# Optimization experiments

Measured on AMD Instinct MI355X. Metric: run time of the kernel, lower is better.

The kernel has to match this reference:

```python
import jax, jax.numpy as jnp
import numpy as np

B, L, ENC, DEC, ATT = 256, 196, 2048, 512, 512


def setup_inputs() -> dict:
    key = jax.random.key(0)
    ks = jax.random.split(key, 10)
    s = lambda d: 1.0 / np.sqrt(d)
    return {
        "x": jax.random.normal(ks[0], (B, L, ENC), dtype=jnp.float32),
        "h": jax.random.normal(ks[1], (B, DEC), dtype=jnp.float32),
        "W_enc": jax.random.uniform(ks[2], (ENC, ATT), jnp.float32, -s(ENC), s(ENC)),
        "b_enc": jax.random.uniform(ks[3], (ATT,), jnp.float32, -s(ENC), s(ENC)),
        "W_dec": jax.random.uniform(ks[4], (DEC, ATT), jnp.float32, -s(DEC), s(DEC)),
        "b_dec": jax.random.uniform(ks[5], (ATT,), jnp.float32, -s(DEC), s(DEC)),
        "W_full": jax.random.uniform(ks[6], (ATT, 1), jnp.float32, -s(ATT), s(ATT)),
        "b_full": jax.random.uniform(ks[7], (1,), jnp.float32, -s(ATT), s(ATT)),
        "W_beta": jax.random.uniform(ks[8], (DEC, 1), jnp.float32, -s(DEC), s(DEC)),
        "b_beta": jax.random.uniform(ks[9], (1,), jnp.float32, -s(DEC), s(DEC)),
    }


def reference(x, h, W_enc, b_enc, W_dec, b_dec, W_full, b_full, W_beta, b_beta):
    # x: [B, L, ENC], h: [B, DEC]
    att1 = jnp.einsum("blc,ca->bla", x, W_enc) + b_enc          # [B, L, ATT]
    att2 = h @ W_dec + b_dec                                     # [B, ATT]
    att = (jax.nn.relu(att1 + att2[:, None, :]) @ W_full)[..., 0] + b_full  # [B, L]
    alpha = jax.nn.softmax(att, axis=-1)                         # [B, L]
    z = jnp.einsum("bl,blc->bc", alpha, x)                       # [B, ENC]
    gate_beta = jax.nn.sigmoid(h @ W_beta + b_beta)              # [B, 1]
    return gate_beta * z, alpha
```

## Files before the change

### kernel.cpp

```cpp
#include <hip/hip_runtime.h>
#include <hip/hip_bf16.h>
#include <cstdint>

#define B_   256
#define L_   196
#define ENC_ 2048
#define DEC_ 512
#define ATT_ 512
#define M_TOT (B_*L_)

typedef short short8 __attribute__((ext_vector_type(8)));
typedef float f32x16 __attribute__((ext_vector_type(16)));

__device__ __forceinline__ unsigned short f2bf(float f) {
    union { float f; unsigned u; } v; v.f = f;
    unsigned u = v.u;
    return (unsigned short)((u + 0x7FFFu + ((u >> 16) & 1u)) >> 16);
}

__device__ __forceinline__ void gl_lds16(const void* g, void* l) {
    __builtin_amdgcn_global_load_lds((const __attribute__((address_space(1))) unsigned int*)g,
                                     (__attribute__((address_space(3))) unsigned int*)l,
                                     16, 0, 0);
}

__global__ void k_transpose(const float* __restrict__ W, unsigned short* __restrict__ WT) {
    __shared__ float S[32*33];
    const int k0 = blockIdx.x * 32, n0 = blockIdx.y * 32;
    const int t  = threadIdx.x;
    const int c31 = t & 31, q = t >> 5;
#pragma unroll
    for (int i = 0; i < 4; ++i) {
        int kl = q + i*8;
        S[c31*33 + kl] = W[(size_t)(k0+kl)*ATT_ + n0 + c31];
    }
    __syncthreads();
#pragma unroll
    for (int i = 0; i < 4; ++i) {
        int nn = q + i*8;
        WT[(size_t)(n0+nn)*ENC_ + k0 + c31] = f2bf(S[nn*33 + c31]);
    }
}

__global__ void k_prep2(const float* __restrict__ h, const float* __restrict__ Wdec,
                        const float* __restrict__ bdec, const float* __restrict__ benc,
                        const float* __restrict__ Wbeta, const float* __restrict__ bbeta,
                        float* __restrict__ att2c, float* __restrict__ gate) {
    const int b = blockIdx.x, t = threadIdx.x;
    __shared__ float hs[DEC_];
    __shared__ float pr[4];
    hs[t]       = h[(size_t)b*DEC_ + t];
    hs[t + 256] = h[(size_t)b*DEC_ + t + 256];
    __syncthreads();
    float a0 = 0.f, a1 = 0.f;
    for (int k = 0; k < DEC_; ++k) {
        float hk = hs[k];
        a0 = fmaf(hk, Wdec[(size_t)k*ATT_ + t],       a0);
        a1 = fmaf(hk, Wdec[(size_t)k*ATT_ + t + 256], a1);
    }
    att2c[(size_t)b*ATT_ + t]       = a0 + bdec[t]       + benc[t];
    att2c[(size_t)b*ATT_ + t + 256] = a1 + bdec[t + 256] + benc[t + 256];
    float p = hs[t]*Wbeta[t] + hs[t+256]*Wbeta[t+256];
#pragma unroll
    for (int mask = 32; mask; mask >>= 1) p += __shfl_xor(p, mask, 64);
    if ((t & 63) == 0) pr[t >> 6] = p;
    __syncthreads();
    if (t == 0) gate[b] = 1.f / (1.f + __expf(-(pr[0]+pr[1]+pr[2]+pr[3] + bbeta[0])));
}

__global__ __launch_bounds__(256, 2) void k_gemm(
        const float* __restrict__ x, const unsigned short* __restrict__ WT,
        const float* __restrict__ att2c, const float* __restrict__ Wfull,
        float* __restrict__ att) {
    __shared__ alignas(16) unsigned short Ab[2][64*32];
    __shared__ alignas(16) unsigned short Bb[2][512*32];
    __shared__ float att_ws[4][64];

    const int tid   = threadIdx.x;
    const int wave  = tid >> 6;
    const int lane  = tid & 63;
    const int lane31 = lane & 31;
    const int laneh  = lane >> 5;
    const int m0 = blockIdx.x * 64;

    f32x16 acc[2][4];
#pragma unroll
    for (int i = 0; i < 2; ++i)
#pragma unroll
        for (int j = 0; j < 4; ++j)
#pragma unroll
            for (int r = 0; r < 16; ++r) acc[i][j][r] = 0.f;

    int boff[8];
#pragma unroll
    for (int j = 0; j < 8; ++j) {
        int c  = (wave*8 + j)*64 + lane;
        int n  = c >> 2;
        int kc = (c & 3) ^ ((n >> 1) & 3);
        boff[j] = n*ENC_ + kc*8;
    }
    const int ar = tid >> 2, g = tid & 3;
    const int achunk = ar*4 + (g ^ ((ar >> 1) & 3));
    const float* xrow = x + (size_t)(m0 + ar)*ENC_ + g*8;

#pragma unroll
    for (int j = 0; j < 8; ++j)
        gl_lds16(WT + boff[j], (void*)&Bb[0][(wave*8 + j)*512]);
    float4 pa = *(const float4*)(xrow);
    float4 pb = *(const float4*)(xrow + 4);
    {
        short8 w;
        w[0] = f2bf(pa.x); w[1] = f2bf(pa.y); w[2] = f2bf(pa.z); w[3] = f2bf(pa.w);
        w[4] = f2bf(pb.x); w[5] = f2bf(pb.y); w[6] = f2bf(pb.z); w[7] = f2bf(pb.w);
        *(short8*)&Ab[0][achunk*8] = w;
    }

    for (int k0 = 0; k0 < ENC_; k0 += 32) {
        const int cur = (k0 >> 5) & 1, nxt = cur ^ 1;
        __syncthreads();
        const bool more = (k0 + 32) < ENC_;
        if (more) {
#pragma unroll
            for (int j = 0; j < 8; ++j)
                gl_lds16(WT + boff[j] + (k0 + 32), (void*)&Bb[nxt][(wave*8 + j)*512]);
            pa = *(const float4*)(xrow + k0 + 32);
            pb = *(const float4*)(xrow + k0 + 36);
        }
#pragma unroll
        for (int ks = 0; ks < 2; ++ks) {
            short8 a[2], bf[4];
#pragma unroll
            for (int mi = 0; mi < 2; ++mi) {
                int m  = mi*32 + lane31;
                int ch = m*4 + ((ks*2 + laneh) ^ ((m >> 1) & 3));
                a[mi] = *(const short8*)&Ab[cur][ch*8];
            }
#pragma unroll
            for (int ni = 0; ni < 4; ++ni) {
                int n  = wave*128 + ni*32 + lane31;
                int ch = n*4 + ((ks*2 + laneh) ^ ((n >> 1) & 3));
                bf[ni] = *(const short8*)&Bb[cur][ch*8];
            }
#pragma unroll
            for (int mi = 0; mi < 2; ++mi)
#pragma unroll
                for (int ni = 0; ni < 4; ++ni)
                    acc[mi][ni] = __builtin_amdgcn_mfma_f32_32x32x16_bf16(
                                      a[mi], bf[ni], acc[mi][ni], 0, 0, 0);
        }
        if (more) {
            short8 w;
            w[0] = f2bf(pa.x); w[1] = f2bf(pa.y); w[2] = f2bf(pa.z); w[3] = f2bf(pa.w);
            w[4] = f2bf(pb.x); w[5] = f2bf(pb.y); w[6] = f2bf(pb.z); w[7] = f2bf(pb.w);
            *(short8*)&Ab[nxt][achunk*8] = w;
        }
    }

    float* epi = (float*)&Bb[0][0];
    {
        const int b0i = m0 / L_;
        const int b1i = (m0 + 63) / L_;
        epi[tid]        = Wfull[tid];
        epi[256 + tid]  = Wfull[256 + tid];
        epi[512 + tid]  = att2c[(size_t)b0i*ATT_ + tid];
        epi[768 + tid]  = att2c[(size_t)b0i*ATT_ + 256 + tid];
        epi[1024 + tid] = att2c[(size_t)b1i*ATT_ + tid];
        epi[1280 + tid] = att2c[(size_t)b1i*ATT_ + 256 + tid];
    }
    __syncthreads();
    const int split = (m0 / L_ + 1) * L_;
#pragma unroll
    for (int mi = 0; mi < 2; ++mi) {
#pragma unroll
        for (int reg = 0; reg < 16; ++reg) {
            int r32  = (reg & 3) + 8*(reg >> 2) + 4*laneh;
            int mloc = mi*32 + r32;
            int off  = (m0 + mloc >= split) ? 1024 : 512;
            float v = 0.f;
#pragma unroll
            for (int ni = 0; ni < 4; ++ni) {
                int n = wave*128 + ni*32 + lane31;
                float tv = acc[mi][ni][reg] + epi[off + n];
                v = fmaf(fmaxf(tv, 0.f), epi[n], v);
            }
#pragma unroll
            for (int mask = 16; mask; mask >>= 1) v += __shfl_xor(v, mask, 64);
            if (lane31 == 0) att_ws[wave][mloc] = v;
        }
    }
    __syncthreads();
    if (tid < 64)
        att[m0 + tid] = att_ws[0][tid] + att_ws[1][tid] + att_ws[2][tid] + att_ws[3][tid];
}

__global__ __launch_bounds__(256) void k_softz(
        const float* __restrict__ att, const float* __restrict__ x,
        const float* __restrict__ gate, float* __restrict__ out) {
    const int b = blockIdx.x, s = blockIdx.y, t = threadIdx.x;
    __shared__ float sa[L_];
    __shared__ float red[8];
    const int wid = t >> 6, lane = t & 63;
    float v = (t < L_) ? att[b*L_ + t] : -1e30f;
    float m = v;
#pragma unroll
    for (int mask = 32; mask; mask >>= 1) m = fmaxf(m, __shfl_xor(m, mask, 64));
    if (lane == 0) red[wid] = m;
    __syncthreads();
    m = fmaxf(fmaxf(red[0], red[1]), fmaxf(red[2], red[3]));
    float e = (t < L_) ? __expf(v - m) : 0.f;
    float sum = e;
#pragma unroll
    for (int mask = 32; mask; mask >>= 1) sum += __shfl_xor(sum, mask, 64);
    if (lane == 0) red[4 + wid] = sum;
    __syncthreads();
    sum = red[4] + red[5] + red[6] + red[7];
    float alpha = e / sum;
    if (t < L_) {
        sa[t] = alpha;
        if (s == 0) out[(size_t)B_*ENC_ + (size_t)b*L_ + t] = alpha;
    }
    __syncthreads();
    const float* xb = x + (size_t)b*L_*ENC_ + s*1024 + t*4;
    float4 z = {0.f, 0.f, 0.f, 0.f};
#pragma unroll 7
    for (int l = 0; l < L_; ++l) {
        float a = sa[l];
        float4 u = *(const float4*)(xb + (size_t)l*ENC_);
        z.x = fmaf(a, u.x, z.x); z.y = fmaf(a, u.y, z.y);
        z.z = fmaf(a, u.z, z.z); z.w = fmaf(a, u.w, z.w);
    }
    const float g = gate[b];
    float4 o; o.x = g*z.x; o.y = g*z.y; o.z = g*z.z; o.w = g*z.w;
    *(float4*)(out + (size_t)b*ENC_ + s*1024 + t*4) = o;
}

extern "C" void kernel_launch(void* const* d_in, const int* in_sizes, int n_in,
                              void* d_out, int out_size, void* d_ws, size_t ws_size,
                              hipStream_t stream) {
    const float* x      = (const float*)d_in[0];
    const float* h      = (const float*)d_in[1];
    const float* W_enc  = (const float*)d_in[2];
    const float* b_enc  = (const float*)d_in[3];
    const float* W_dec  = (const float*)d_in[4];
    const float* b_dec  = (const float*)d_in[5];
    const float* W_full = (const float*)d_in[6];
    const float* W_beta = (const float*)d_in[8];
    const float* b_beta = (const float*)d_in[9];
    float* out = (float*)d_out;

    char* ws = (char*)d_ws;
    unsigned short* WT = (unsigned short*)ws;
    float* att2c  = (float*)(ws + 2*1024*1024);
    float* gate   = (float*)(ws + 2*1024*1024 + 512*1024);
    float* attbuf = (float*)(ws + 2*1024*1024 + 512*1024 + 1024);

    k_transpose<<<dim3(ENC_/32, ATT_/32), 256, 0, stream>>>(W_enc, WT);
    k_prep2   <<<B_, 256, 0, stream>>>(h, W_dec, b_dec, b_enc, W_beta, b_beta, att2c, gate);
    k_gemm    <<<M_TOT/64, 256, 0, stream>>>(x, WT, att2c, W_full, attbuf);
    k_softz   <<<dim3(B_, 2), 256, 0, stream>>>(attbuf, x, gate, out);
}
```

Before: 767.0 us.

## Deepen GEMM prefetch to two stages and software-pipeline softmax-z reduction

The GEMM main loop is rewritten with a manually unrolled macro that keeps two k-steps of x prefetched in registers. All LDS fragments are loaded up front, and the next weight tile is issued by global_load_lds into the buffer just consumed. Barriers are replaced by hand-written s_waitcnt vmcnt/lgkmcnt plus s_barrier so loads stay in flight across iterations. The softz kernel reverses batch block order, likely to reuse x still in cache from the end of the GEMM, and double-buffers seven rows of loads in registers. The cost is more register pressure and fragile hand-tuned waitcnt counts that could race if the compiler reorders memory operations.

```diff
diff --git a/kernel.cpp b/kernel.cpp
--- a/kernel.cpp
+++ b/kernel.cpp
@@ -103,58 +103,73 @@
     const int achunk = ar*4 + (g ^ ((ar >> 1) & 3));
     const float* xrow = x + (size_t)(m0 + ar)*ENC_ + g*8;
 
+    float4 pa0, pb0, pa1, pb1;
 #pragma unroll
     for (int j = 0; j < 8; ++j)
         gl_lds16(WT + boff[j], (void*)&Bb[0][(wave*8 + j)*512]);
-    float4 pa = *(const float4*)(xrow);
-    float4 pb = *(const float4*)(xrow + 4);
+    pa0 = *(const float4*)(xrow);
+    pb0 = *(const float4*)(xrow + 4);
+#pragma unroll
+    for (int j = 0; j < 8; ++j)
+        gl_lds16(WT + boff[j] + 32, (void*)&Bb[1][(wave*8 + j)*512]);
+    pa1 = *(const float4*)(xrow + 32);
+    pb1 = *(const float4*)(xrow + 36);
     {
         short8 w;
-        w[0] = f2bf(pa.x); w[1] = f2bf(pa.y); w[2] = f2bf(pa.z); w[3] = f2bf(pa.w);
-        w[4] = f2bf(pb.x); w[5] = f2bf(pb.y); w[6] = f2bf(pb.z); w[7] = f2bf(pb.w);
+        w[0] = f2bf(pa0.x); w[1] = f2bf(pa0.y); w[2] = f2bf(pa0.z); w[3] = f2bf(pa0.w);
+        w[4] = f2bf(pb0.x); w[5] = f2bf(pb0.y); w[6] = f2bf(pb0.z); w[7] = f2bf(pb0.w);
         *(short8*)&Ab[0][achunk*8] = w;
     }
-
-    for (int k0 = 0; k0 < ENC_; k0 += 32) {
-        const int cur = (k0 >> 5) & 1, nxt = cur ^ 1;
-        __syncthreads();
-        const bool more = (k0 + 32) < ENC_;
-        if (more) {
-#pragma unroll
-            for (int j = 0; j < 8; ++j)
-                gl_lds16(WT + boff[j] + (k0 + 32), (void*)&Bb[nxt][(wave*8 + j)*512]);
-            pa = *(const float4*)(xrow + k0 + 32);
-            pb = *(const float4*)(xrow + k0 + 36);
-        }
-#pragma unroll
-        for (int ks = 0; ks < 2; ++ks) {
-            short8 a[2], bf[4];
-#pragma unroll
-            for (int mi = 0; mi < 2; ++mi) {
-                int m  = mi*32 + lane31;
-                int ch = m*4 + ((ks*2 + laneh) ^ ((m >> 1) & 3));
-                a[mi] = *(const short8*)&Ab[cur][ch*8];
-            }
-#pragma unroll
-            for (int ni = 0; ni < 4; ++ni) {
-                int n  = wave*128 + ni*32 + lane31;
-                int ch = n*4 + ((ks*2 + laneh) ^ ((n >> 1) & 3));
-                bf[ni] = *(const short8*)&Bb[cur][ch*8];
-            }
-#pragma unroll
-            for (int mi = 0; mi < 2; ++mi)
-#pragma unroll
-                for (int ni = 0; ni < 4; ++ni)
-                    acc[mi][ni] = __builtin_amdgcn_mfma_f32_32x32x16_bf16(
-                                      a[mi], bf[ni], acc[mi][ni], 0, 0, 0);
-        }
-        if (more) {
-            short8 w;
-            w[0] = f2bf(pa.x); w[1] = f2bf(pa.y); w[2] = f2bf(pa.z); w[3] = f2bf(pa.w);
-            w[4] = f2bf(pb.x); w[5] = f2bf(pb.y); w[6] = f2bf(pb.z); w[7] = f2bf(pb.w);
-            *(short8*)&Ab[nxt][achunk*8] = w;
-        }
-    }
+    asm volatile("s_waitcnt vmcnt(10) lgkmcnt(0)\n\ts_barrier" ::: "memory");
+
+#define GEMM_ITER(K, XW0, XW1, XR0, XR1)                                              \
+{                                                                                     \
+    const int cur = (K) & 1, nxt = cur ^ 1;                                           \
+    if ((K) + 2 < 64) {                             \
+        XW0 = *(const float4*)(xrow + ((K)+2)*32);                                    \
+        XW1 = *(const float4*)(xrow + ((K)+2)*32 + 4);                                \
+    }                                                                                 \
+    short8 a[2][2], bf[2][4];                                                         \
+    _Pragma("unroll") for (int ks = 0; ks < 2; ++ks) {                                \
+        _Pragma("unroll") for (int mi = 0; mi < 2; ++mi) {                            \
+            int m  = mi*32 + lane31;                                                  \
+            int ch = m*4 + ((ks*2 + laneh) ^ ((m >> 1) & 3));                         \
+            a[ks][mi] = *(const short8*)&Ab[cur][ch*8];                               \
+        }                                                                             \
+        _Pragma("unroll") for (int ni = 0; ni < 4; ++ni) {                            \
+            int n  = wave*128 + ni*32 + lane31;                                       \
+            int ch = n*4 + ((ks*2 + laneh) ^ ((n >> 1) & 3));                         \
+            bf[ks][ni] = *(const short8*)&Bb[cur][ch*8];                              \
+        }                                                                             \
+    }                                                                                 \
+           \
+    asm volatile("s_waitcnt lgkmcnt(0)" ::: "memory");                                \
+    if ((K) + 2 < 64) {                                                               \
+        _Pragma("unroll") for (int j = 0; j < 8; ++j)                                 \
+            gl_lds16(WT + boff[j] + ((K)+2)*32, (void*)&Bb[cur][(wave*8 + j)*512]);   \
+    }                                                                                 \
+    _Pragma("unroll") for (int ks = 0; ks < 2; ++ks)                                  \
+        _Pragma("unroll") for (int mi = 0; mi < 2; ++mi)                              \
+            _Pragma("unroll") for (int ni = 0; ni < 4; ++ni)                          \
+                acc[mi][ni] = __builtin_amdgcn_mfma_f32_32x32x16_bf16(                \
+                                  a[ks][mi], bf[ks][ni], acc[mi][ni], 0, 0, 0);       \
+    if ((K) + 1 < 64) {               \
+        short8 w;                                                                     \
+        w[0] = f2bf(XR0.x); w[1] = f2bf(XR0.y); w[2] = f2bf(XR0.z); w[3] = f2bf(XR0.w);\
+        w[4] = f2bf(XR1.x); w[5] = f2bf(XR1.y); w[6] = f2bf(XR1.z); w[7] = f2bf(XR1.w);\
+        *(short8*)&Ab[nxt][achunk*8] = w;                                             \
+    }                                                                                 \
+    if ((K) < 62)                                                                     \
+        asm volatile("s_waitcnt vmcnt(10) lgkmcnt(0)\n\ts_barrier" ::: "memory");     \
+    else                                                                              \
+        asm volatile("s_waitcnt vmcnt(0) lgkmcnt(0)\n\ts_barrier" ::: "memory");      \
+}
+
+    for (int K = 0; K < 64; K += 2) {
+        GEMM_ITER(K,     pa0, pb0, pa1, pb1)
+        GEMM_ITER(K + 1, pa1, pb1, pa0, pb0)
+    }
+#undef GEMM_ITER
 
     float* epi = (float*)&Bb[0][0];
     {
@@ -196,7 +211,8 @@
 __global__ __launch_bounds__(256) void k_softz(
         const float* __restrict__ att, const float* __restrict__ x,
         const float* __restrict__ gate, float* __restrict__ out) {
-    const int b = blockIdx.x, s = blockIdx.y, t = threadIdx.x;
+    const int b = (B_ - 1) - (int)blockIdx.x;
+    const int s = blockIdx.y, t = threadIdx.x;
     __shared__ float sa[L_];
     __shared__ float red[8];
     const int wid = t >> 6, lane = t & 63;
@@ -222,15 +238,30 @@
     __syncthreads();
     const float* xb = x + (size_t)b*L_*ENC_ + s*1024 + t*4;
     float4 z = {0.f, 0.f, 0.f, 0.f};
-#pragma unroll 7
-    for (int l = 0; l < L_; ++l) {
-        float a = sa[l];
-        float4 u = *(const float4*)(xb + (size_t)l*ENC_);
-        z.x = fmaf(a, u.x, z.x); z.y = fmaf(a, u.y, z.y);
-        z.z = fmaf(a, u.z, z.z); z.w = fmaf(a, u.w, z.w);
-    }
-    const float g = gate[b];
-    float4 o; o.x = g*z.x; o.y = g*z.y; o.z = g*z.z; o.w = g*z.w;
+    float4 u[7], w[7];
+#pragma unroll
+    for (int i = 0; i < 7; ++i) u[i] = *(const float4*)(xb + (size_t)i*ENC_);
+    for (int l0 = 0; l0 < 183; l0 += 7) {
+#pragma unroll
+        for (int i = 0; i < 7; ++i)
+            w[i] = *(const float4*)(xb + (size_t)(l0 + 7 + i)*ENC_);
+#pragma unroll
+        for (int i = 0; i < 7; ++i) {
+            float a_ = sa[l0 + i];
+            z.x = fmaf(a_, u[i].x, z.x); z.y = fmaf(a_, u[i].y, z.y);
+            z.z = fmaf(a_, u[i].z, z.z); z.w = fmaf(a_, u[i].w, z.w);
+        }
+#pragma unroll
+        for (int i = 0; i < 7; ++i) u[i] = w[i];
+    }
+#pragma unroll
+    for (int i = 0; i < 7; ++i) {
+        float a_ = sa[189 + i];
+        z.x = fmaf(a_, u[i].x, z.x); z.y = fmaf(a_, u[i].y, z.y);
+        z.z = fmaf(a_, u[i].z, z.z); z.w = fmaf(a_, u[i].w, z.w);
+    }
+    const float gt = gate[b];
+    float4 o; o.x = gt*z.x; o.y = gt*z.y; o.z = gt*z.z; o.w = gt*z.w;
     *(float4*)(out + (size_t)b*ENC_ + s*1024 + t*4) = o;
 }
 
```

After: 762.0 us. About the same (-0.7%).
